# Performance work log

Hardware: AMD Instinct MI355X
Metric: run time of the kernel (lower is better)

Reference implementation:

```python
import jax, jax.numpy as jnp
import numpy as np

H, W = 512, 1024
NUM_CLASSES = 19
N_THING = 8
CENTER_THRESHOLD = 0.1
NMS_KERNEL = 7
KEEP_K = 128


def setup_inputs() -> dict:
    key = jax.random.key(0)
    k1, k2, k3 = jax.random.split(key, 3)
    return {
        "semantic_logits": jax.random.normal(k1, (1, H, W, NUM_CLASSES), jnp.float32),
        "center_heatmap": jax.random.uniform(k2, (H, W, 1), dtype=jnp.float32),
        "center_offsets": jax.random.normal(k3, (H, W, 2), jnp.float32) * 8.0,
        "thing_class_ids": jnp.arange(N_THING, dtype=jnp.int32),
    }


def _nms_heatmap(center_heatmap):
    # threshold, then keep only local maxima of a k x k max-pool (zero-padded;
    # -inf init is equivalent since thresholded values are >= 0)
    hm = jnp.where(center_heatmap > CENTER_THRESHOLD, center_heatmap, 0.0)  # [H,W,1]
    pooled = jax.lax.reduce_window(hm, -jnp.inf, jax.lax.max,
                                   (NMS_KERNEL, NMS_KERNEL, 1), (1, 1, 1), 'SAME')
    hm = jnp.where(pooled == hm, hm, 0.0)
    return hm[..., 0]  # [H,W]


def reference(semantic_logits, center_heatmap, center_offsets, thing_class_ids):
    # semantic prediction [H,W] (batch=1, like the TF merge path)
    semantic = jnp.argmax(semantic_logits, axis=-1).astype(jnp.int32)[0]
    thing_mask = (semantic[..., None] == thing_class_ids[None, None, :]).any(-1)  # [H,W] bool

    hm = _nms_heatmap(center_heatmap)                     # [H,W]
    scores, idx = jax.lax.top_k(hm.reshape(-1), KEEP_K)   # fixed-K centers
    valid = scores > 0.0                                  # [K]
    cy = (idx // W).astype(jnp.float32)
    cx = (idx % W).astype(jnp.float32)
    centers = jnp.stack([cy, cx], axis=-1)                # [K,2] (y,x)

    # center-per-pixel = pixel coord + predicted offset
    yy, xx = jnp.meshgrid(jnp.arange(H, dtype=jnp.float32),
                          jnp.arange(W, dtype=jnp.float32), indexing='ij')
    cpp = (jnp.stack([yy, xx], axis=-1) + center_offsets).reshape(-1, 2)  # [HW,2]

    # squared euclidean distance (argmin-equivalent to tf.norm), matmul form
    d2 = ((centers ** 2).sum(-1)[:, None]
          - 2.0 * centers @ cpp.T
          + (cpp ** 2).sum(-1)[None, :])                  # [K,HW]
    d2 = jnp.where(valid[:, None], d2, jnp.inf)           # mask padded centers
    assign = jnp.argmin(d2, axis=0).reshape(H, W)         # closest center index

    instance_seg = (assign.astype(jnp.int32) + 1) * thing_mask.astype(jnp.int32)
    score_map = scores[assign] * thing_mask.astype(jnp.float32)
    return instance_seg, hm, score_map, semantic
```

## Files before the change

kernel.cpp:

```cpp
#include <hip/hip_runtime.h>

#define HH 512
#define WW 1024
#define HWSZ (HH*WW)
#define NCLS 19
#define KEEP 128
#define CTHR 0.1f
#define NBLK 512
#define NRED 16
#define SEGPB 32
#define GSLOT 192
#define TAGMAGIC 0x5A17EC0Du
typedef unsigned int u32;
typedef unsigned long long u64;

static __device__ __forceinline__ int key_bin2k(u64 k) {
    unsigned u = (unsigned)(k >> 32);
    if (u >= 0x3F000000u) {
        int b = 1024 + (int)((u - 0x3F000000u) >> 13);
        return b > 2047 ? 2047 : b;
    }
    return (int)(u >> 21);
}

static __device__ __forceinline__ int lds_push(int* cnt, bool want, int lane, u64 lmask_lt) {
    u64 mask = __ballot(want);
    int pos = -1;
    if (mask) {
        int leader = __builtin_ctzll(mask);
        int bpos = 0;
        if (lane == leader) bpos = atomicAdd(cnt, (int)__popcll(mask));
        bpos = __shfl(bpos, leader);
        if (want) pos = bpos + (int)__popcll(mask & lmask_lt);
    }
    return pos;
}

static __device__ __forceinline__ void bitonic_lds(u64* b, int m, int tid) {
    for (int kk = 2; kk <= m; kk <<= 1) {
        for (int j = kk >> 1; j; j >>= 1) {
            for (int i = tid; i < m; i += 256) {
                int ixj = i ^ j;
                if (ixj > i) {
                    bool desc = ((i & kk) == 0);
                    u64 a = b[i], c = b[ixj];
                    if ((a < c) == desc) { b[i] = c; b[ixj] = a; }
                }
            }
            __syncthreads();
        }
    }
}

static __device__ __forceinline__ void bitonic256_reg(u64* ov, int tid) {
    u64 a = ov[tid];
    __syncthreads();
    for (int kk = 2; kk <= 256; kk <<= 1) {
        bool desc = ((tid & kk) == 0);
        for (int j = kk >> 1; j; j >>= 1) {
            u64 b;
            if (j >= 64) {
                ov[tid] = a; __syncthreads();
                b = ov[tid ^ j]; __syncthreads();
            } else {
                b = __shfl_xor(a, j);
            }
            bool up = ((tid & j) == 0);
            bool keepMax = (up == desc);
            a = keepMax ? (a > b ? a : b) : (a < b ? a : b);
        }
    }
    ov[tid] = a;
    __syncthreads();
}

static __device__ __forceinline__ int cutoff2k(unsigned* hist, unsigned* cs, int tid,
                                               int* s_bin, int* s_K) {
    if (tid == 0) *s_bin = 2048;
    unsigned c = 0;
#pragma unroll
    for (int i = 0; i < 8; i++) c += hist[tid * 8 + i];
    cs[tid] = c;
    __syncthreads();
    for (int d = 1; d < 256; d <<= 1) {
        unsigned v = cs[tid];
        unsigned w = (tid + d < 256) ? cs[tid + d] : 0u;
        __syncthreads();
        cs[tid] = v + w;
        __syncthreads();
    }
    if (tid == 0) *s_K = (int)cs[0] < KEEP ? (int)cs[0] : KEEP;
    __syncthreads();
    int K = *s_K;
    unsigned above = (tid < 255) ? cs[tid + 1] : 0u;
    if (K > 0 && above < (unsigned)K && (unsigned)K <= cs[tid]) {
        unsigned acc = above;
        for (int b = 7; b >= 0; b--) {
            unsigned h = hist[tid * 8 + b];
            if (acc + h >= (unsigned)K) { *s_bin = tid * 8 + b; break; }
            acc += h;
        }
    }
    __syncthreads();
    return *s_bin;
}

__global__ void nms_kernel(const float* __restrict__ hm_in, float* __restrict__ hm_out,
                           u64* __restrict__ keys, int* __restrict__ blkcnt, int maxpb)
{
    const int TX = 64, TY = 16;
    __shared__ float sin_[TY + 6][TX + 6];
    __shared__ float shm[TY + 6][TX];
    __shared__ u64 lkeys[TX * TY];
    __shared__ int lcnt;

    if (threadIdx.x == 0) lcnt = 0;
    int bx = blockIdx.x & 15, by = blockIdx.x >> 4;
    int ox = bx * TX, oy = by * TY;

    for (int i = threadIdx.x; i < (TY + 6) * (TX + 6); i += blockDim.x) {
        int ly = i / (TX + 6), lx = i % (TX + 6);
        int gy = oy + ly - 3, gx = ox + lx - 3;
        float v = 0.f;
        if (gy >= 0 && gy < HH && gx >= 0 && gx < WW) {
            float t = hm_in[gy * WW + gx];
            v = (t > CTHR) ? t : 0.f;
        }
        sin_[ly][lx] = v;
    }
    __syncthreads();
    for (int i = threadIdx.x; i < (TY + 6) * TX; i += blockDim.x) {
        int ly = i / TX, lx = i % TX;
        float m = sin_[ly][lx];
#pragma unroll
        for (int d = 1; d < 7; d++) m = fmaxf(m, sin_[ly][lx + d]);
        shm[ly][lx] = m;
    }
    __syncthreads();
    for (int i = threadIdx.x; i < TY * TX; i += blockDim.x) {
        int ly = i / TX, lx = i % TX;
        float m = shm[ly][lx];
#pragma unroll
        for (int d = 1; d < 7; d++) m = fmaxf(m, shm[ly + d][lx]);
        float c = sin_[ly + 3][lx + 3];
        float o = (m == c) ? c : 0.f;
        int gy = oy + ly, gx = ox + lx;
        hm_out[gy * WW + gx] = o;
        if (o > 0.f) {
            int pos = atomicAdd(&lcnt, 1);
            lkeys[pos] = ((u64)__float_as_uint(o) << 32) |
                         (u64)(0xFFFFFFFFu - (unsigned)(gy * WW + gx));
        }
    }
    __syncthreads();
    int n = lcnt < maxpb ? lcnt : maxpb;
    if (threadIdx.x == 0) blkcnt[blockIdx.x] = n;
    for (int i = threadIdx.x; i < n; i += blockDim.x)
        keys[(size_t)i * NBLK + blockIdx.x] = lkeys[i];
}

__global__ void __launch_bounds__(256) reduce_select_kernel(
        const u64* __restrict__ keys, const int* __restrict__ blkcnt, int maxpb,
        u64* __restrict__ gtop, u32* __restrict__ gcnt, u32* __restrict__ tag2arr,
        float4* __restrict__ centers)
{
    __shared__ __align__(16) char smem[33792];
    __shared__ int scnt2[SEGPB];
    __shared__ int s_m, s_bin, s_K, s_out;

    int tid = threadIdx.x, lane = tid & 63;
    u64 lmask_lt = (1ull << lane) - 1ull;

    u64* kbuf = (u64*)smem;
    unsigned* hist = (unsigned*)(smem + 24576);
    unsigned* cs   = (unsigned*)(smem + 32768);

    if (blockIdx.x < NRED) {
        int r = blockIdx.x, g0 = r * SEGPB;
        if (tid < SEGPB) {
            int c = blkcnt[g0 + tid];
            scnt2[tid] = c < 0 ? 0 : (c > maxpb ? maxpb : c);
        }
        if (tid == 0) s_m = 0;
        { uint4* h4 = (uint4*)hist; for (int i = tid; i < 512; i += 256) h4[i] = make_uint4(0,0,0,0); }
        __syncthreads();
        int mxc = 0;
        for (int j = 0; j < SEGPB; j++) { int c = scnt2[j]; mxc = c > mxc ? c : mxc; }
        int nslots = SEGPB * mxc;

        for (int base = 0; base < nslots; base += 1024) {
            u64 kv[4]; bool pv[4];
#pragma unroll
            for (int u = 0; u < 4; u++) {
                int i = base + u * 256 + tid;
                int sg = i & (SEGPB - 1), sl = i >> 5;
                pv[u] = (i < nslots) && (sl < scnt2[sg]);
                kv[u] = pv[u] ? keys[(size_t)sl * NBLK + (g0 + sg)] : 0ull;
            }
#pragma unroll
            for (int u = 0; u < 4; u++)
                if (pv[u]) atomicAdd(&hist[key_bin2k(kv[u])], 1u);
        }
        __syncthreads();
        int cb = cutoff2k(hist, cs, tid, &s_bin, &s_K);

        for (int base = 0; base < nslots; base += 1024) {
#pragma unroll
            for (int u = 0; u < 4; u++) {
                int i = base + u * 256 + tid;
                int sg = i & (SEGPB - 1), sl = i >> 5;
                bool pv = (i < nslots) && (sl < scnt2[sg]);
                u64 kv = pv ? keys[(size_t)sl * NBLK + (g0 + sg)] : 0ull;
                bool want = pv && key_bin2k(kv) >= cb;
                int pos = lds_push(&s_m, want, lane, lmask_lt);
                if (want) kbuf[pos] = kv;
            }
        }
        __syncthreads();
        int n = s_m;
        if (n <= GSLOT) {
            for (int i = tid; i < n; i += 256) gtop[r * GSLOT + i] = kbuf[i];
            if (tid == 0) s_out = n;
        } else {
            int m = 256; while (m < n) m <<= 1;
            for (int i = tid; i < m; i += 256) if (i >= n) kbuf[i] = 0ull;
            __syncthreads();
            if (m == 256) bitonic256_reg(kbuf, tid); else bitonic_lds(kbuf, m, tid);
            if (tid < KEEP) gtop[r * GSLOT + tid] = kbuf[tid];
            if (tid == 0) s_out = KEEP;
        }
        __syncthreads();
        if (tid == 0) {
            __hip_atomic_store(&gcnt[r], (u32)s_out, __ATOMIC_RELAXED, __HIP_MEMORY_SCOPE_AGENT);
            __hip_atomic_store(&tag2arr[r], TAGMAGIC, __ATOMIC_RELEASE, __HIP_MEMORY_SCOPE_AGENT);
        }
        return;
    }

    if (tid < NRED) {
        while (__hip_atomic_load(&tag2arr[tid], __ATOMIC_RELAXED,
                                 __HIP_MEMORY_SCOPE_AGENT) != TAGMAGIC)
            __builtin_amdgcn_s_sleep(8);
    }
    __syncthreads();
    if (tid == 0) __threadfence();
    __syncthreads();
    if (tid < NRED) {
        int c = (int)gcnt[tid];
        scnt2[tid] = c < 0 ? 0 : (c > GSLOT ? GSLOT : c);
    }
    if (tid == 0) s_m = 0;
    { uint4* h4 = (uint4*)hist; for (int i = tid; i < 512; i += 256) h4[i] = make_uint4(0,0,0,0); }
    __syncthreads();

    const int nslots = NRED * GSLOT;
    for (int base = 0; base < nslots; base += 1024) {
        u64 kv[4]; bool pv[4];
#pragma unroll
        for (int u = 0; u < 4; u++) {
            int i = base + u * 256 + tid;
            int b = i / GSLOT, j = i - b * GSLOT;
            pv[u] = (j < scnt2[b]);
            kv[u] = pv[u] ? gtop[i] : 0ull;
        }
#pragma unroll
        for (int u = 0; u < 4; u++)
            if (pv[u]) atomicAdd(&hist[key_bin2k(kv[u])], 1u);
    }
    __syncthreads();
    int cb = cutoff2k(hist, cs, tid, &s_bin, &s_K);

    for (int base = 0; base < nslots; base += 1024) {
#pragma unroll
        for (int u = 0; u < 4; u++) {
            int i = base + u * 256 + tid;
            int b = i / GSLOT, j = i - b * GSLOT;
            bool pv = (j < scnt2[b]);
            u64 kv = pv ? gtop[i] : 0ull;
            bool want = pv && key_bin2k(kv) >= cb;
            int pos = lds_push(&s_m, want, lane, lmask_lt);
            if (want) kbuf[pos] = kv;
        }
    }
    __syncthreads();
    int n = s_m;
    int m = 256; while (m < n) m <<= 1;
    for (int i = tid; i < m; i += 256) if (i >= n) kbuf[i] = 0ull;
    __syncthreads();
    if (m == 256) bitonic256_reg(kbuf, tid); else bitonic_lds(kbuf, m, tid);

    if (tid < KEEP) {
        u64 k64 = kbuf[tid];
        float sc_, cy, cx, a;
        if (k64 == 0ull) { sc_ = 0.f; cy = 0.f; cx = 0.f; a = 0.f; }
        else {
            sc_ = __uint_as_float((unsigned)(k64 >> 32));
            unsigned idx = 0xFFFFFFFFu - (unsigned)(k64 & 0xFFFFFFFFu);
            cy = (float)(idx / WW);
            cx = (float)(idx % WW);
            a = cy * cy + cx * cx;
        }
        centers[tid] = make_float4(cy, cx, a, sc_);
    }
    if (tid < NRED)
        __hip_atomic_store(&tag2arr[tid], 0u, __ATOMIC_RELAXED, __HIP_MEMORY_SCOPE_AGENT);
}

__global__ void __launch_bounds__(256) assign_kernel(
        const float* __restrict__ logits, const float* __restrict__ offs,
        const int* __restrict__ thing_ids, int n_thing,
        const float4* __restrict__ centers, float* __restrict__ out)
{
    __shared__ float4 sc[KEEP];
    __shared__ float4 skept[KEEP];
    __shared__ int   skidx[KEEP];
    __shared__ float slog[256 * NCLS];
    __shared__ float sred[16];
    __shared__ float ured[4];
    __shared__ int   wcnt[4];
    __shared__ int   s_nkept;
    __shared__ int   sids[32];

    int tid = threadIdx.x;
    if (tid < KEEP) sc[tid] = centers[tid];
    if (tid < n_thing) sids[tid] = thing_ids[tid];

    int bx = blockIdx.x & 63;
    int by = blockIdx.x >> 6;
    int lr = tid >> 4, lc = tid & 15;
    int gy = by * 16 + lr, gx = bx * 16 + lc;
    int p  = gy * WW + gx;

    {
        const float4* src4 = (const float4*)(logits + ((size_t)(by * 16) * WW + bx * 16) * NCLS);
        float4* dst4 = (float4*)slog;
        for (int i = tid; i < 16 * 76; i += 256) {
            int r = i / 76, cidx = i % 76;
            dst4[i] = src4[(size_t)r * 4864 + cidx];
        }
    }

    float2 off2 = ((const float2*)offs)[p];
    float py = __fadd_rn((float)gy, off2.x);
    float px = __fadd_rn((float)gx, off2.y);

    float ymn = py, ymx = py, xmn = px, xmx = px;
    for (int d = 32; d; d >>= 1) {
        ymn = fminf(ymn, __shfl_xor(ymn, d));
        ymx = fmaxf(ymx, __shfl_xor(ymx, d));
        xmn = fminf(xmn, __shfl_xor(xmn, d));
        xmx = fmaxf(xmx, __shfl_xor(xmx, d));
    }
    if ((tid & 63) == 0) {
        int w = tid >> 6;
        sred[w * 4 + 0] = ymn; sred[w * 4 + 1] = ymx;
        sred[w * 4 + 2] = xmn; sred[w * 4 + 3] = xmx;
    }
    __syncthreads();

    ymn = fminf(fminf(sred[0], sred[4]), fminf(sred[8],  sred[12]));
    ymx = fmaxf(fmaxf(sred[1], sred[5]), fmaxf(sred[9],  sred[13]));
    xmn = fminf(fminf(sred[2], sred[6]), fminf(sred[10], sred[14]));
    xmx = fmaxf(fmaxf(sred[3], sred[7]), fmaxf(sred[11], sred[15]));

    float L = INFINITY, U = INFINITY;
    bool valid = false;
    if (tid < KEEP) {
        float4 c4 = sc[tid];
        valid = (c4.w > 0.f);
        if (valid) {
            float dyl = fmaxf(fmaxf(ymn - c4.x, c4.x - ymx), 0.f);
            float dxl = fmaxf(fmaxf(xmn - c4.y, c4.y - xmx), 0.f);
            L = dyl * dyl + dxl * dxl;
            float dyu = fmaxf(fabsf(c4.x - ymn), fabsf(c4.x - ymx));
            float dxu = fmaxf(fabsf(c4.y - xmn), fabsf(c4.y - xmx));
            U = dyu * dyu + dxu * dxu;
        }
    }
    float u = U;
    for (int d = 32; d; d >>= 1) u = fminf(u, __shfl_xor(u, d));
    if ((tid & 63) == 0) ured[tid >> 6] = u;
    __syncthreads();
    float Umin = fminf(fminf(ured[0], ured[1]), fminf(ured[2], ured[3]));

    bool keep = valid && (L <= Umin + 8.0f);
    u64 mask = __ballot(keep);
    int lane = tid & 63;
    int prefix = __popcll(mask & ((1ull << lane) - 1ull));
    if (lane == 0) wcnt[tid >> 6] = __popcll(mask);
    __syncthreads();
    int base = (tid >> 6) == 1 ? wcnt[0] : 0;
    if (keep) { skept[base + prefix] = sc[tid]; skidx[base + prefix] = tid; }
    if (tid == 0) s_nkept = wcnt[0] + wcnt[1];
    __syncthreads();

    const float* l = slog + tid * NCLS;
    float best = l[0];
    int cls = 0;
#pragma unroll
    for (int cc = 1; cc < NCLS; cc++) {
        float v = l[cc];
        if (v > best) { best = v; cls = cc; }
    }
    bool thing = false;
    for (int j = 0; j < n_thing; j++) thing = thing || (cls == sids[j]);

    float b = __fadd_rn(__fmul_rn(py, py), __fmul_rn(px, px));

    float bestd = INFINITY;
    int bi = -1;
    int nk = s_nkept;
    for (int k = 0; k < nk; k++) {
        float4 c4 = skept[k];
        float m  = __fmaf_rn(c4.y, px, __fmul_rn(c4.x, py));
        float d2 = __fadd_rn(__fsub_rn(c4.z, __fadd_rn(m, m)), b);
        if (d2 < bestd) { bestd = d2; bi = k; }
    }

    float inst, smap;
    if (bi < 0) { inst = thing ? 1.f : 0.f; smap = 0.f; }
    else {
        inst = thing ? (float)(skidx[bi] + 1) : 0.f;
        smap = thing ? skept[bi].w : 0.f;
    }
    out[p] = inst;
    out[2 * HWSZ + p] = smap;
    out[3 * HWSZ + p] = (float)cls;
}

extern "C" void kernel_launch(void* const* d_in, const int* in_sizes, int n_in,
                              void* d_out, int out_size, void* d_ws, size_t ws_size,
                              hipStream_t stream) {
    const float* logits = (const float*)d_in[0];
    const float* heat   = (const float*)d_in[1];
    const float* offs   = (const float*)d_in[2];
    const int*   tids   = (const int*)d_in[3];
    int n_thing = in_sizes[3];
    if (n_thing > 32) n_thing = 32;

    float* out = (float*)d_out;
    char* ws = (char*)d_ws;
    u32* tag2arr = (u32*)ws;
    u32* gcnt    = (u32*)(ws + 2048);
    int* blkcnt  = (int*)(ws + 4096);
    float4* centers = (float4*)(ws + 8192);
    u64* gtop = (u64*)(ws + 16384);
    long long avail = (long long)ws_size - 65536;
    int maxpb = (int)(avail / (NBLK * 8));
    if (maxpb > 96) maxpb = 96;
    if (maxpb < 16) maxpb = 16;
    u64* keys = (u64*)(ws + 65536);

    nms_kernel<<<dim3(NBLK), dim3(256), 0, stream>>>(heat, out + HWSZ, keys, blkcnt, maxpb);
    reduce_select_kernel<<<dim3(NRED + 1), dim3(256), 0, stream>>>(
        keys, blkcnt, maxpb, gtop, gcnt, tag2arr, centers);
    assign_kernel<<<dim3(2048), dim3(256), 0, stream>>>(
        logits, offs, tids, n_thing, centers, out);
}
```

Before: 42.69 us.

## Fuse center selection with pixel assignment in one persistent grid using flag waits

Merges the reduce/select kernel and the assign kernel into one 1024-block launch. Each block handles two pixel tiles and starts loading logits and offsets for its first tile, then spins on a per-block flag until block NRED has published the 128 centers. The flags and tags are reset inside the NMS kernel. This removes one kernel launch and the gap between select and assign, overlapping the serial top-k selection with memory loads. In exchange, correctness depends on all 1024 blocks being co-resident or scheduled after the producer blocks, and every block must wait on the serial selection before it can do its first tile's assignment.

```diff
diff --git a/kernel.cpp b/kernel.cpp
--- a/kernel.cpp
+++ b/kernel.cpp
@@ -10,6 +10,7 @@
 #define NRED 16
 #define SEGPB 32
 #define GSLOT 192
+#define GRID2 1024
 #define TAGMAGIC 0x5A17EC0Du
 typedef unsigned int u32;
 typedef unsigned long long u64;
@@ -106,7 +107,8 @@
 }
 
 __global__ void nms_kernel(const float* __restrict__ hm_in, float* __restrict__ hm_out,
-                           u64* __restrict__ keys, int* __restrict__ blkcnt, int maxpb)
+                           u64* __restrict__ keys, int* __restrict__ blkcnt, int maxpb,
+                           u32* __restrict__ wflags, u32* __restrict__ tag2arr)
 {
     const int TX = 64, TY = 16;
     __shared__ float sin_[TY + 6][TX + 6];
@@ -114,6 +116,12 @@
     __shared__ u64 lkeys[TX * TY];
     __shared__ int lcnt;
 
+    if (blockIdx.x < 4) {
+        for (int i = threadIdx.x; i < 1024; i += 256)
+            wflags[blockIdx.x * 1024 + i] = 0u;
+    } else if (blockIdx.x == 4) {
+        if (threadIdx.x < NRED) tag2arr[threadIdx.x] = 0u;
+    }
     if (threadIdx.x == 0) lcnt = 0;
     int bx = blockIdx.x & 15, by = blockIdx.x >> 4;
     int ox = bx * TX, oy = by * TY;
@@ -159,24 +167,39 @@
         keys[(size_t)i * NBLK + blockIdx.x] = lkeys[i];
 }
 
-__global__ void __launch_bounds__(256) reduce_select_kernel(
+__global__ void __launch_bounds__(256) fused_kernel(
+        const float* __restrict__ logits, const float* __restrict__ offs,
+        const int* __restrict__ thing_ids, int n_thing,
         const u64* __restrict__ keys, const int* __restrict__ blkcnt, int maxpb,
         u64* __restrict__ gtop, u32* __restrict__ gcnt, u32* __restrict__ tag2arr,
-        float4* __restrict__ centers)
+        u32* __restrict__ wflags, float4* __restrict__ centers, float* __restrict__ out)
 {
     __shared__ __align__(16) char smem[33792];
     __shared__ int scnt2[SEGPB];
-    __shared__ int s_m, s_bin, s_K, s_out;
-
-    int tid = threadIdx.x, lane = tid & 63;
+    __shared__ int s_m, s_bin, s_K, s_out, s_nkept;
+    __shared__ float sred[16];
+    __shared__ float ured[4];
+    __shared__ int wcnt[4];
+    __shared__ int sids[32];
+
+    int bid = blockIdx.x;
+    int tid = threadIdx.x, lane = tid & 63, wid = tid >> 6;
     u64 lmask_lt = (1ull << lane) - 1ull;
+
+    if (tid < n_thing) sids[tid] = thing_ids[tid];
 
     u64* kbuf = (u64*)smem;
     unsigned* hist = (unsigned*)(smem + 24576);
     unsigned* cs   = (unsigned*)(smem + 32768);
-
-    if (blockIdx.x < NRED) {
-        int r = blockIdx.x, g0 = r * SEGPB;
+    float*  slog  = (float*)smem;
+    float4* sc    = (float4*)(smem + 19456);
+    float4* skept = (float4*)(smem + 21504);
+    int*    skidx = (int*)(smem + 23552);
+
+    float c16x = 0.f, c16y = 0.f, c16z = 0.f, c16w = 0.f;
+
+    if (bid < NRED) {
+        int r = bid, g0 = r * SEGPB;
         if (tid < SEGPB) {
             int c = blkcnt[g0 + tid];
             scnt2[tid] = c < 0 ? 0 : (c > maxpb ? maxpb : c);
@@ -234,198 +257,195 @@
             __hip_atomic_store(&gcnt[r], (u32)s_out, __ATOMIC_RELAXED, __HIP_MEMORY_SCOPE_AGENT);
             __hip_atomic_store(&tag2arr[r], TAGMAGIC, __ATOMIC_RELEASE, __HIP_MEMORY_SCOPE_AGENT);
         }
-        return;
-    }
-
-    if (tid < NRED) {
-        while (__hip_atomic_load(&tag2arr[tid], __ATOMIC_RELAXED,
-                                 __HIP_MEMORY_SCOPE_AGENT) != TAGMAGIC)
-            __builtin_amdgcn_s_sleep(8);
-    }
-    __syncthreads();
-    if (tid == 0) __threadfence();
-    __syncthreads();
-    if (tid < NRED) {
-        int c = (int)gcnt[tid];
-        scnt2[tid] = c < 0 ? 0 : (c > GSLOT ? GSLOT : c);
-    }
-    if (tid == 0) s_m = 0;
-    { uint4* h4 = (uint4*)hist; for (int i = tid; i < 512; i += 256) h4[i] = make_uint4(0,0,0,0); }
-    __syncthreads();
-
-    const int nslots = NRED * GSLOT;
-    for (int base = 0; base < nslots; base += 1024) {
-        u64 kv[4]; bool pv[4];
-#pragma unroll
-        for (int u = 0; u < 4; u++) {
-            int i = base + u * 256 + tid;
-            int b = i / GSLOT, j = i - b * GSLOT;
-            pv[u] = (j < scnt2[b]);
-            kv[u] = pv[u] ? gtop[i] : 0ull;
-        }
-#pragma unroll
-        for (int u = 0; u < 4; u++)
-            if (pv[u]) atomicAdd(&hist[key_bin2k(kv[u])], 1u);
-    }
-    __syncthreads();
-    int cb = cutoff2k(hist, cs, tid, &s_bin, &s_K);
-
-    for (int base = 0; base < nslots; base += 1024) {
-#pragma unroll
-        for (int u = 0; u < 4; u++) {
-            int i = base + u * 256 + tid;
-            int b = i / GSLOT, j = i - b * GSLOT;
-            bool pv = (j < scnt2[b]);
-            u64 kv = pv ? gtop[i] : 0ull;
-            bool want = pv && key_bin2k(kv) >= cb;
-            int pos = lds_push(&s_m, want, lane, lmask_lt);
-            if (want) kbuf[pos] = kv;
-        }
-    }
-    __syncthreads();
-    int n = s_m;
-    int m = 256; while (m < n) m <<= 1;
-    for (int i = tid; i < m; i += 256) if (i >= n) kbuf[i] = 0ull;
-    __syncthreads();
-    if (m == 256) bitonic256_reg(kbuf, tid); else bitonic_lds(kbuf, m, tid);
-
-    if (tid < KEEP) {
-        u64 k64 = kbuf[tid];
-        float sc_, cy, cx, a;
-        if (k64 == 0ull) { sc_ = 0.f; cy = 0.f; cx = 0.f; a = 0.f; }
+    } else if (bid == NRED) {
+        if (tid < NRED) {
+            while (__hip_atomic_load(&tag2arr[tid], __ATOMIC_RELAXED,
+                                     __HIP_MEMORY_SCOPE_AGENT) != TAGMAGIC)
+                __builtin_amdgcn_s_sleep(8);
+        }
+        __syncthreads();
+        if (tid == 0) __threadfence();
+        __syncthreads();
+        if (tid < NRED) {
+            int c = (int)gcnt[tid];
+            scnt2[tid] = c < 0 ? 0 : (c > GSLOT ? GSLOT : c);
+        }
+        if (tid == 0) s_m = 0;
+        { uint4* h4 = (uint4*)hist; for (int i = tid; i < 512; i += 256) h4[i] = make_uint4(0,0,0,0); }
+        __syncthreads();
+
+        const int nslots = NRED * GSLOT;
+        for (int base = 0; base < nslots; base += 1024) {
+            u64 kv[4]; bool pv[4];
+#pragma unroll
+            for (int u = 0; u < 4; u++) {
+                int i = base + u * 256 + tid;
+                int b = i / GSLOT, j = i - b * GSLOT;
+                pv[u] = (j < scnt2[b]);
+                kv[u] = pv[u] ? gtop[i] : 0ull;
+            }
+#pragma unroll
+            for (int u = 0; u < 4; u++)
+                if (pv[u]) atomicAdd(&hist[key_bin2k(kv[u])], 1u);
+        }
+        __syncthreads();
+        int cb = cutoff2k(hist, cs, tid, &s_bin, &s_K);
+
+        for (int base = 0; base < nslots; base += 1024) {
+#pragma unroll
+            for (int u = 0; u < 4; u++) {
+                int i = base + u * 256 + tid;
+                int b = i / GSLOT, j = i - b * GSLOT;
+                bool pv = (j < scnt2[b]);
+                u64 kv = pv ? gtop[i] : 0ull;
+                bool want = pv && key_bin2k(kv) >= cb;
+                int pos = lds_push(&s_m, want, lane, lmask_lt);
+                if (want) kbuf[pos] = kv;
+            }
+        }
+        __syncthreads();
+        int n = s_m;
+        int m = 256; while (m < n) m <<= 1;
+        for (int i = tid; i < m; i += 256) if (i >= n) kbuf[i] = 0ull;
+        __syncthreads();
+        if (m == 256) bitonic256_reg(kbuf, tid); else bitonic_lds(kbuf, m, tid);
+
+        if (tid < KEEP) {
+            u64 k64 = kbuf[tid];
+            if (k64 != 0ull) {
+                c16w = __uint_as_float((unsigned)(k64 >> 32));
+                unsigned idx = 0xFFFFFFFFu - (unsigned)(k64 & 0xFFFFFFFFu);
+                c16x = (float)(idx / WW);
+                c16y = (float)(idx % WW);
+                c16z = c16x * c16x + c16y * c16y;
+            }
+            centers[tid] = make_float4(c16x, c16y, c16z, c16w);
+        }
+        __syncthreads();
+        if (tid == 0) __threadfence();
+        __syncthreads();
+#pragma unroll
+        for (int k = 0; k < 4; k++)
+            __hip_atomic_store(&wflags[(size_t)(tid + k * 256) * 4], TAGMAGIC,
+                               __ATOMIC_RELAXED, __HIP_MEMORY_SCOPE_AGENT);
+    }
+
+    for (int j = 0; j < 2; j++) {
+        int tile = bid + GRID2 * j;
+        __syncthreads();
+        int tbx = tile & 63, tby = tile >> 6;
+        int lr = tid >> 4, lc = tid & 15;
+        int gy = tby * 16 + lr, gx = tbx * 16 + lc;
+        int p = gy * WW + gx;
+
+        {
+            const float4* src4 = (const float4*)(logits + ((size_t)(tby * 16) * WW + tbx * 16) * NCLS);
+            float4* dst4 = (float4*)slog;
+            for (int i = tid; i < 16 * 76; i += 256) {
+                int r = i / 76, cidx = i % 76;
+                dst4[i] = src4[(size_t)r * 4864 + cidx];
+            }
+        }
+
+        float2 off2 = ((const float2*)offs)[p];
+        float py = __fadd_rn((float)gy, off2.x);
+        float px = __fadd_rn((float)gx, off2.y);
+
+        float ymn = py, ymx = py, xmn = px, xmx = px;
+        for (int d = 32; d; d >>= 1) {
+            ymn = fminf(ymn, __shfl_xor(ymn, d));
+            ymx = fmaxf(ymx, __shfl_xor(ymx, d));
+            xmn = fminf(xmn, __shfl_xor(xmn, d));
+            xmx = fmaxf(xmx, __shfl_xor(xmx, d));
+        }
+        if (lane == 0) {
+            sred[wid * 4 + 0] = ymn; sred[wid * 4 + 1] = ymx;
+            sred[wid * 4 + 2] = xmn; sred[wid * 4 + 3] = xmx;
+        }
+
+        if (j == 0) {
+            if (tid == 0 && bid != NRED) {
+                while (__hip_atomic_load(&wflags[(size_t)bid * 4], __ATOMIC_RELAXED,
+                                         __HIP_MEMORY_SCOPE_AGENT) != TAGMAGIC)
+                    __builtin_amdgcn_s_sleep(8);
+                __threadfence();
+            }
+            __syncthreads();
+            if (tid < KEEP) {
+                if (bid == NRED) sc[tid] = make_float4(c16x, c16y, c16z, c16w);
+                else             sc[tid] = centers[tid];
+            }
+        }
+        __syncthreads();
+
+        float lymn = fminf(fminf(sred[0], sred[4]), fminf(sred[8],  sred[12]));
+        float lymx = fmaxf(fmaxf(sred[1], sred[5]), fmaxf(sred[9],  sred[13]));
+        float lxmn = fminf(fminf(sred[2], sred[6]), fminf(sred[10], sred[14]));
+        float lxmx = fmaxf(fmaxf(sred[3], sred[7]), fmaxf(sred[11], sred[15]));
+
+        float L = INFINITY, U = INFINITY;
+        bool valid = false;
+        if (tid < KEEP) {
+            float4 c4 = sc[tid];
+            valid = (c4.w > 0.f);
+            if (valid) {
+                float dyl = fmaxf(fmaxf(lymn - c4.x, c4.x - lymx), 0.f);
+                float dxl = fmaxf(fmaxf(lxmn - c4.y, c4.y - lxmx), 0.f);
+                L = dyl * dyl + dxl * dxl;
+                float dyu = fmaxf(fabsf(c4.x - lymn), fabsf(c4.x - lymx));
+                float dxu = fmaxf(fabsf(c4.y - lxmn), fabsf(c4.y - lxmx));
+                U = dyu * dyu + dxu * dxu;
+            }
+        }
+        float u = U;
+        for (int d = 32; d; d >>= 1) u = fminf(u, __shfl_xor(u, d));
+        if (lane == 0) ured[wid] = u;
+        __syncthreads();
+        float Umin = fminf(fminf(ured[0], ured[1]), fminf(ured[2], ured[3]));
+
+        bool keep = valid && (L <= Umin + 8.0f);
+        u64 kmask = __ballot(keep);
+        int prefix = __popcll(kmask & lmask_lt);
+        if (lane == 0) wcnt[wid] = __popcll(kmask);
+        __syncthreads();
+        int base = (wid == 1) ? wcnt[0] : 0;
+        if (keep) { skept[base + prefix] = sc[tid]; skidx[base + prefix] = tid; }
+        if (tid == 0) s_nkept = wcnt[0] + wcnt[1];
+        __syncthreads();
+
+        const float* l = slog + tid * NCLS;
+        float best = l[0];
+        int cls = 0;
+#pragma unroll
+        for (int cc = 1; cc < NCLS; cc++) {
+            float v = l[cc];
+            if (v > best) { best = v; cls = cc; }
+        }
+        bool thing = false;
+        for (int jj = 0; jj < n_thing; jj++) thing = thing || (cls == sids[jj]);
+
+        float b = __fadd_rn(__fmul_rn(py, py), __fmul_rn(px, px));
+
+        float bestd = INFINITY;
+        int bi = -1;
+        int nk = s_nkept;
+        for (int k = 0; k < nk; k++) {
+            float4 c4 = skept[k];
+            float m  = __fmaf_rn(c4.y, px, __fmul_rn(c4.x, py));
+            float d2 = __fadd_rn(__fsub_rn(c4.z, __fadd_rn(m, m)), b);
+            if (d2 < bestd) { bestd = d2; bi = k; }
+        }
+
+        float inst, smap;
+        if (bi < 0) { inst = thing ? 1.f : 0.f; smap = 0.f; }
         else {
-            sc_ = __uint_as_float((unsigned)(k64 >> 32));
-            unsigned idx = 0xFFFFFFFFu - (unsigned)(k64 & 0xFFFFFFFFu);
-            cy = (float)(idx / WW);
-            cx = (float)(idx % WW);
-            a = cy * cy + cx * cx;
-        }
-        centers[tid] = make_float4(cy, cx, a, sc_);
-    }
-    if (tid < NRED)
-        __hip_atomic_store(&tag2arr[tid], 0u, __ATOMIC_RELAXED, __HIP_MEMORY_SCOPE_AGENT);
-}
-
-__global__ void __launch_bounds__(256) assign_kernel(
-        const float* __restrict__ logits, const float* __restrict__ offs,
-        const int* __restrict__ thing_ids, int n_thing,
-        const float4* __restrict__ centers, float* __restrict__ out)
-{
-    __shared__ float4 sc[KEEP];
-    __shared__ float4 skept[KEEP];
-    __shared__ int   skidx[KEEP];
-    __shared__ float slog[256 * NCLS];
-    __shared__ float sred[16];
-    __shared__ float ured[4];
-    __shared__ int   wcnt[4];
-    __shared__ int   s_nkept;
-    __shared__ int   sids[32];
-
-    int tid = threadIdx.x;
-    if (tid < KEEP) sc[tid] = centers[tid];
-    if (tid < n_thing) sids[tid] = thing_ids[tid];
-
-    int bx = blockIdx.x & 63;
-    int by = blockIdx.x >> 6;
-    int lr = tid >> 4, lc = tid & 15;
-    int gy = by * 16 + lr, gx = bx * 16 + lc;
-    int p  = gy * WW + gx;
-
-    {
-        const float4* src4 = (const float4*)(logits + ((size_t)(by * 16) * WW + bx * 16) * NCLS);
-        float4* dst4 = (float4*)slog;
-        for (int i = tid; i < 16 * 76; i += 256) {
-            int r = i / 76, cidx = i % 76;
-            dst4[i] = src4[(size_t)r * 4864 + cidx];
-        }
-    }
-
-    float2 off2 = ((const float2*)offs)[p];
-    float py = __fadd_rn((float)gy, off2.x);
-    float px = __fadd_rn((float)gx, off2.y);
-
-    float ymn = py, ymx = py, xmn = px, xmx = px;
-    for (int d = 32; d; d >>= 1) {
-        ymn = fminf(ymn, __shfl_xor(ymn, d));
-        ymx = fmaxf(ymx, __shfl_xor(ymx, d));
-        xmn = fminf(xmn, __shfl_xor(xmn, d));
-        xmx = fmaxf(xmx, __shfl_xor(xmx, d));
-    }
-    if ((tid & 63) == 0) {
-        int w = tid >> 6;
-        sred[w * 4 + 0] = ymn; sred[w * 4 + 1] = ymx;
-        sred[w * 4 + 2] = xmn; sred[w * 4 + 3] = xmx;
-    }
-    __syncthreads();
-
-    ymn = fminf(fminf(sred[0], sred[4]), fminf(sred[8],  sred[12]));
-    ymx = fmaxf(fmaxf(sred[1], sred[5]), fmaxf(sred[9],  sred[13]));
-    xmn = fminf(fminf(sred[2], sred[6]), fminf(sred[10], sred[14]));
-    xmx = fmaxf(fmaxf(sred[3], sred[7]), fmaxf(sred[11], sred[15]));
-
-    float L = INFINITY, U = INFINITY;
-    bool valid = false;
-    if (tid < KEEP) {
-        float4 c4 = sc[tid];
-        valid = (c4.w > 0.f);
-        if (valid) {
-            float dyl = fmaxf(fmaxf(ymn - c4.x, c4.x - ymx), 0.f);
-            float dxl = fmaxf(fmaxf(xmn - c4.y, c4.y - xmx), 0.f);
-            L = dyl * dyl + dxl * dxl;
-            float dyu = fmaxf(fabsf(c4.x - ymn), fabsf(c4.x - ymx));
-            float dxu = fmaxf(fabsf(c4.y - xmn), fabsf(c4.y - xmx));
-            U = dyu * dyu + dxu * dxu;
-        }
-    }
-    float u = U;
-    for (int d = 32; d; d >>= 1) u = fminf(u, __shfl_xor(u, d));
-    if ((tid & 63) == 0) ured[tid >> 6] = u;
-    __syncthreads();
-    float Umin = fminf(fminf(ured[0], ured[1]), fminf(ured[2], ured[3]));
-
-    bool keep = valid && (L <= Umin + 8.0f);
-    u64 mask = __ballot(keep);
-    int lane = tid & 63;
-    int prefix = __popcll(mask & ((1ull << lane) - 1ull));
-    if (lane == 0) wcnt[tid >> 6] = __popcll(mask);
-    __syncthreads();
-    int base = (tid >> 6) == 1 ? wcnt[0] : 0;
-    if (keep) { skept[base + prefix] = sc[tid]; skidx[base + prefix] = tid; }
-    if (tid == 0) s_nkept = wcnt[0] + wcnt[1];
-    __syncthreads();
-
-    const float* l = slog + tid * NCLS;
-    float best = l[0];
-    int cls = 0;
-#pragma unroll
-    for (int cc = 1; cc < NCLS; cc++) {
-        float v = l[cc];
-        if (v > best) { best = v; cls = cc; }
-    }
-    bool thing = false;
-    for (int j = 0; j < n_thing; j++) thing = thing || (cls == sids[j]);
-
-    float b = __fadd_rn(__fmul_rn(py, py), __fmul_rn(px, px));
-
-    float bestd = INFINITY;
-    int bi = -1;
-    int nk = s_nkept;
-    for (int k = 0; k < nk; k++) {
-        float4 c4 = skept[k];
-        float m  = __fmaf_rn(c4.y, px, __fmul_rn(c4.x, py));
-        float d2 = __fadd_rn(__fsub_rn(c4.z, __fadd_rn(m, m)), b);
-        if (d2 < bestd) { bestd = d2; bi = k; }
-    }
-
-    float inst, smap;
-    if (bi < 0) { inst = thing ? 1.f : 0.f; smap = 0.f; }
-    else {
-        inst = thing ? (float)(skidx[bi] + 1) : 0.f;
-        smap = thing ? skept[bi].w : 0.f;
-    }
-    out[p] = inst;
-    out[2 * HWSZ + p] = smap;
-    out[3 * HWSZ + p] = (float)cls;
+            inst = thing ? (float)(skidx[bi] + 1) : 0.f;
+            smap = thing ? skept[bi].w : 0.f;
+        }
+        out[p] = inst;
+        out[2 * HWSZ + p] = smap;
+        out[3 * HWSZ + p] = (float)cls;
+    }
 }
 
 extern "C" void kernel_launch(void* const* d_in, const int* in_sizes, int n_in,
@@ -444,16 +464,17 @@
     u32* gcnt    = (u32*)(ws + 2048);
     int* blkcnt  = (int*)(ws + 4096);
     float4* centers = (float4*)(ws + 8192);
-    u64* gtop = (u64*)(ws + 16384);
+    u32* wflags  = (u32*)(ws + 16384);
+    u64* gtop    = (u64*)(ws + 32768);
     long long avail = (long long)ws_size - 65536;
     int maxpb = (int)(avail / (NBLK * 8));
     if (maxpb > 96) maxpb = 96;
     if (maxpb < 16) maxpb = 16;
     u64* keys = (u64*)(ws + 65536);
 
-    nms_kernel<<<dim3(NBLK), dim3(256), 0, stream>>>(heat, out + HWSZ, keys, blkcnt, maxpb);
-    reduce_select_kernel<<<dim3(NRED + 1), dim3(256), 0, stream>>>(
-        keys, blkcnt, maxpb, gtop, gcnt, tag2arr, centers);
-    assign_kernel<<<dim3(2048), dim3(256), 0, stream>>>(
-        logits, offs, tids, n_thing, centers, out);
-}
+    nms_kernel<<<dim3(NBLK), dim3(256), 0, stream>>>(heat, out + HWSZ, keys, blkcnt, maxpb,
+                                                     wflags, tag2arr);
+    fused_kernel<<<dim3(GRID2), dim3(256), 0, stream>>>(
+        logits, offs, tids, n_thing, keys, blkcnt, maxpb,
+        gtop, gcnt, tag2arr, wflags, centers, out);
+}
```

Result: slower. 55.97 us (+31.1%).
